# Kernel optimization log

Hardware: AMD Instinct MI355X
Metric: run time of the kernel (lower is better)

Reference implementation:

```python
import jax, jax.numpy as jnp
import numpy as np

HIDDEN = 1024
HEADS = 16
HEAD_DIM = HIDDEN // HEADS
SEQ = 2048
BATCH = 2


def setup_inputs() -> dict:
    key = jax.random.key(0)
    ks = jax.random.split(key, 11)
    s = 1.0 / np.sqrt(HIDDEN)
    inp = {
        'query': jax.random.normal(ks[0], (SEQ, BATCH, HIDDEN), jnp.float32),
        'key': jax.random.normal(ks[1], (SEQ, BATCH, HIDDEN), jnp.float32),
        'value': jax.random.normal(ks[2], (SEQ, BATCH, HIDDEN), jnp.float32),
        'Wq': jax.random.normal(ks[3], (HIDDEN, HIDDEN), jnp.float32) * s,
        'bq': jnp.zeros((HIDDEN,), jnp.float32),
        'Wk': jax.random.normal(ks[4], (HIDDEN, HIDDEN), jnp.float32) * s,
        'bk': jnp.zeros((HIDDEN,), jnp.float32),
        'Wv': jax.random.normal(ks[5], (HIDDEN, HIDDEN), jnp.float32) * s,
        'bv': jnp.zeros((HIDDEN,), jnp.float32),
        'Wo': jax.random.normal(ks[6], (HIDDEN, HIDDEN), jnp.float32) * s,
        'bo': jnp.zeros((HIDDEN,), jnp.float32),
    }
    return inp


def reference(query, key, value, Wq, bq, Wk, bk, Wv, bv, Wo, bo):
    # Linear layers: torch Linear computes x @ W.T + b
    S, B, _ = query.shape
    q = (query @ Wq.T + bq).reshape(S, B, HEADS, HEAD_DIM)
    k = (key @ Wk.T + bk).reshape(S, B, HEADS, HEAD_DIM)
    v = (value @ Wv.T + bv).reshape(S, B, HEADS, HEAD_DIM)
    # -> [B, H, S, D]
    q = jnp.transpose(q, (1, 2, 0, 3))
    k = jnp.transpose(k, (1, 2, 0, 3))
    v = jnp.transpose(v, (1, 2, 0, 3))
    scores = jnp.einsum('bhqd,bhkd->bhqk', q, k) / np.sqrt(HEAD_DIM)
    attn = jax.nn.softmax(scores, axis=-1)  # dropout=0.0 -> identity
    out = jnp.einsum('bhqk,bhkd->bhqd', attn, v)
    out = jnp.transpose(out, (2, 0, 1, 3)).reshape(S, B, HIDDEN)
    out = out @ Wo.T + bo
    return out, attn
```

## Files before the change

### kernel.cpp

```cpp
#include <hip/hip_runtime.h>
#include <hip/hip_bf16.h>
#include <cstdint>
#include <cstddef>

#define SEQLEN 2048
#define NBATCH 2
#define NHEAD  16
#define HDIM   64
#define HID    1024
#define MROWS  4096

typedef __bf16 bf16x8 __attribute__((ext_vector_type(8)));
typedef float f32x4 __attribute__((ext_vector_type(4)));
typedef unsigned short ushort8 __attribute__((ext_vector_type(8)));

#define MFMA16(a, b, c) __builtin_amdgcn_mfma_f32_16x16x32_bf16((a), (b), (c), 0, 0, 0)

#define GLOAD_LDS16(g, l)                                                        \
    __builtin_amdgcn_global_load_lds(                                            \
        (const __attribute__((address_space(1))) void*)(g),                      \
        (__attribute__((address_space(3))) void*)(l), 16, 0, 0)

static __device__ __forceinline__ unsigned int pack_bf16_pair(float lo, float hi) {
    unsigned short a = __builtin_bit_cast(unsigned short, (__bf16)lo);
    unsigned short b = __builtin_bit_cast(unsigned short, (__bf16)hi);
    return ((unsigned int)b << 16) | a;
}

__global__ __launch_bounds__(256) void conv6(
    const float* __restrict__ s0, const float* __restrict__ s1, const float* __restrict__ s2,
    const float* __restrict__ s3, const float* __restrict__ s4, const float* __restrict__ s5,
    unsigned short* __restrict__ Sc)
{
    const int y = blockIdx.y;
    const float* src = (y == 0) ? s0 : (y == 1) ? s1 : (y == 2) ? s2
                     : (y == 3) ? s3 : (y == 4) ? s4 : s5;
    const size_t M1 = 1u << 20;
    unsigned short* dst = (y < 3) ? (Sc + (size_t)y * 4 * M1) : (Sc + 12 * M1 + (size_t)(y - 3) * M1);
    const size_t n = (y < 3) ? 4 * M1 : M1;

    const size_t i = ((size_t)blockIdx.x * 256 + threadIdx.x) * 8;
    if (i >= n) return;
    float4 f0 = *(const float4*)(src + i);
    float4 f1 = *(const float4*)(src + i + 4);
    ushort8 o;
    o[0] = __builtin_bit_cast(unsigned short, (__bf16)f0.x);
    o[1] = __builtin_bit_cast(unsigned short, (__bf16)f0.y);
    o[2] = __builtin_bit_cast(unsigned short, (__bf16)f0.z);
    o[3] = __builtin_bit_cast(unsigned short, (__bf16)f0.w);
    o[4] = __builtin_bit_cast(unsigned short, (__bf16)f1.x);
    o[5] = __builtin_bit_cast(unsigned short, (__bf16)f1.y);
    o[6] = __builtin_bit_cast(unsigned short, (__bf16)f1.z);
    o[7] = __builtin_bit_cast(unsigned short, (__bf16)f1.w);
    *(ushort8*)(dst + i) = o;
}

__global__ __launch_bounds__(256) void wconv(
    const float* __restrict__ Wo, unsigned short* __restrict__ Wob)
{
    const size_t i = ((size_t)blockIdx.x * 256 + threadIdx.x) * 8;
    float4 f0 = *(const float4*)(Wo + i);
    float4 f1 = *(const float4*)(Wo + i + 4);
    ushort8 o;
    o[0] = __builtin_bit_cast(unsigned short, (__bf16)f0.x);
    o[1] = __builtin_bit_cast(unsigned short, (__bf16)f0.y);
    o[2] = __builtin_bit_cast(unsigned short, (__bf16)f0.z);
    o[3] = __builtin_bit_cast(unsigned short, (__bf16)f0.w);
    o[4] = __builtin_bit_cast(unsigned short, (__bf16)f1.x);
    o[5] = __builtin_bit_cast(unsigned short, (__bf16)f1.y);
    o[6] = __builtin_bit_cast(unsigned short, (__bf16)f1.z);
    o[7] = __builtin_bit_cast(unsigned short, (__bf16)f1.w);
    *(ushort8*)(Wob + i) = o;
}

#define GEMM_STAGE(LDSBUF, SRCP)                                                  \
    _Pragma("unroll")                                                             \
    for (int c = 0; c < 4; ++c) {                                                 \
        const int rb = (w << 5) + (c << 3);                                       \
        const int row = rb + (lane >> 3);                                         \
        const unsigned short* src = (SRCP) + (size_t)row * HID + k0               \
                                  + (((lane & 7) ^ ((lane >> 3) & 7)) << 3);      \
        GLOAD_LDS16(src, &LDSBUF[rb * 64]);                                       \
    }

__global__ __launch_bounds__(256) void qkv_gemm(
    const unsigned short* __restrict__ Sc,
    const float* __restrict__ bq, const float* __restrict__ bk, const float* __restrict__ bv,
    unsigned short* __restrict__ Qb, unsigned short* __restrict__ Kb, unsigned short* __restrict__ Vb)
{
    const int z = blockIdx.z;
    const size_t M1 = 1u << 20;
    const unsigned short* A = Sc + (size_t)z * 4 * M1;
    const unsigned short* B = Sc + 12 * M1 + (size_t)z * M1;
    const float* bias = (z == 0) ? bq : (z == 1) ? bk : bv;
    unsigned short* dst = (z == 0) ? Qb : (z == 1) ? Kb : Vb;

    __shared__ unsigned short As[128 * 64];
    __shared__ unsigned short Bs[128 * 64];

    const int t = threadIdx.x, lane = t & 63, w = t >> 6;
    const int wm = w >> 1, wn = w & 1;
    const int bm = blockIdx.x * 128, bn = blockIdx.y * 128;
    const int fr = lane & 15, fg = lane >> 4;

    f32x4 acc[4][4] = {};
    const char* Ac = (const char*)As;
    const char* Bc = (const char*)Bs;

    for (int k0 = 0; k0 < HID; k0 += 64) {
        __syncthreads();
        GEMM_STAGE(As, A + (size_t)bm * HID)
        GEMM_STAGE(Bs, B + (size_t)bn * HID)
        __syncthreads();

        #pragma unroll
        for (int kk = 0; kk < 2; ++kk) {
            bf16x8 a_h[4], b_h[4];
            #pragma unroll
            for (int m = 0; m < 4; ++m) {
                const int row = wm * 64 + m * 16 + fr;
                a_h[m] = *(const bf16x8*)(Ac + (row << 7) + (((kk << 6) | (fg << 4)) ^ ((row & 7) << 4)));
            }
            #pragma unroll
            for (int n = 0; n < 4; ++n) {
                const int row = wn * 64 + n * 16 + fr;
                b_h[n] = *(const bf16x8*)(Bc + (row << 7) + (((kk << 6) | (fg << 4)) ^ ((row & 7) << 4)));
            }
            __builtin_amdgcn_s_setprio(1);
            #pragma unroll
            for (int m = 0; m < 4; ++m)
                #pragma unroll
                for (int n = 0; n < 4; ++n)
                    acc[m][n] = MFMA16(a_h[m], b_h[n], acc[m][n]);
            __builtin_amdgcn_s_setprio(0);
        }
    }

    #pragma unroll
    for (int n = 0; n < 4; ++n) {
        const int gc = bn + wn * 64 + n * 16 + fr;
        const float bb = bias[gc];
        #pragma unroll
        for (int m = 0; m < 4; ++m)
            #pragma unroll
            for (int r = 0; r < 4; ++r) {
                const int gr = bm + wm * 64 + m * 16 + fg * 4 + r;
                *(__bf16*)&dst[(size_t)gr * HID + gc] = (__bf16)(acc[m][n][r] + bb);
            }
    }
}

__global__ __launch_bounds__(256) void vtrans(
    const unsigned short* __restrict__ Vb, unsigned short* __restrict__ Vt)
{
    __shared__ unsigned short T[64][66];
    const int t = threadIdx.x;
    const int s0 = blockIdx.x * 64, h = blockIdx.y, b = blockIdx.z;

    {
        const int s_l = t >> 2, d0 = (t & 3) * 16;
        const unsigned short* src = Vb + (((size_t)(s0 + s_l) * 2 + b) << 10) + (h << 6) + d0;
        *(ushort8*)&T[s_l][d0]     = *(const ushort8*)src;
        *(ushort8*)&T[s_l][d0 + 8] = *(const ushort8*)(src + 8);
    }
    __syncthreads();
    {
        const int d_l = t >> 2, sc = (t & 3) * 16;
        ushort8 o0, o1;
        #pragma unroll
        for (int j = 0; j < 8; ++j) { o0[j] = T[sc + j][d_l]; o1[j] = T[sc + 8 + j][d_l]; }
        unsigned short* dst = Vt + (((size_t)((b << 4) + h) * 64 + d_l) << 11) + s0 + sc;
        *(ushort8*)dst       = o0;
        *(ushort8*)(dst + 8) = o1;
    }
}

__global__ __launch_bounds__(256) void attn2(
    const unsigned short* __restrict__ Qb, const unsigned short* __restrict__ Kb,
    const unsigned short* __restrict__ Vt, float* __restrict__ attn_out,
    unsigned short* __restrict__ Hb)
{
    __shared__ unsigned short Ks[128 * 64];
    __shared__ unsigned short Pl[4 * 32 * 128];

    const int flat = blockIdx.x + (blockIdx.y << 4) + (blockIdx.z << 8);
    const int nf = (flat & 7) * 64 + (flat >> 3);
    const int qblk = nf & 15, h = (nf >> 4) & 15, b = nf >> 8;

    const int t = threadIdx.x, lane = t & 63, w = t >> 6;
    const int fr = lane & 15, fg = lane >> 4;
    const int fg4 = fg << 2, fg16 = fg << 4;
    const int qbase = qblk * 128 + w * 32;
    const float scale = 0.125f;

    bf16x8 qf[2][2];
    #pragma unroll
    for (int mi = 0; mi < 2; ++mi) {
        const int q = qbase + mi * 16 + fr;
        const unsigned short* qp = Qb + (((size_t)q * 2 + b) << 10) + (h << 6);
        qf[mi][0] = *(const bf16x8*)(qp + (fg << 3));
        qf[mi][1] = *(const bf16x8*)(qp + 32 + (fg << 3));
    }

    const char* Ksc = (const char*)Ks;
    char* Plc = (char*)&Pl[w * 4096];

    float lsum[2] = {0.f, 0.f};

    for (int kt = 0; kt < 16; ++kt) {
        __syncthreads();
        #pragma unroll
        for (int c = 0; c < 4; ++c) {
            const int rb = (w << 5) + (c << 3);
            const int row_l = rb + (lane >> 3);
            const unsigned short* src = Kb + (((size_t)((kt << 7) + row_l) * 2 + b) << 10) + (h << 6)
                                         + (((lane & 7) ^ (row_l & 7)) << 3);
            GLOAD_LDS16(src, &Ks[rb * 64]);
        }
        __syncthreads();

        f32x4 s_[2][8] = {};
        __builtin_amdgcn_s_setprio(1);
        #pragma unroll
        for (int n = 0; n < 8; ++n) {
            const int row = (n << 4) + fr;
            const int rx = (row & 7) << 4;
            #pragma unroll
            for (int kk = 0; kk < 2; ++kk) {
                bf16x8 kf = *(const bf16x8*)(Ksc + (row << 7) + (((kk << 6) | fg16) ^ rx));
                s_[0][n] = MFMA16(kf, qf[0][kk], s_[0][n]);
                s_[1][n] = MFMA16(kf, qf[1][kk], s_[1][n]);
            }
        }
        __builtin_amdgcn_s_setprio(0);
        #pragma unroll
        for (int mi = 0; mi < 2; ++mi) {
            float a = 0.f;
            #pragma unroll
            for (int n = 0; n < 8; ++n)
                #pragma unroll
                for (int r = 0; r < 4; ++r)
                    a += __expf(fminf(s_[mi][n][r] * scale, 60.f));
            lsum[mi] += a;
        }
    }

    float inv[2];
    #pragma unroll
    for (int mi = 0; mi < 2; ++mi) {
        float v = lsum[mi];
        v += __shfl_xor(v, 16);
        v += __shfl_xor(v, 32);
        inv[mi] = 1.f / v;
    }

    f32x4 oacc[2][4] = {};
    float* attnB = attn_out + ((size_t)((b << 4) + h) << 22);
    const size_t vhead = (size_t)((b << 4) + h) << 6;

    for (int kt = 0; kt < 16; ++kt) {
        __syncthreads();
        #pragma unroll
        for (int c = 0; c < 4; ++c) {
            const int rb = (w << 5) + (c << 3);
            const int row_l = rb + (lane >> 3);
            const unsigned short* src = Kb + (((size_t)((kt << 7) + row_l) * 2 + b) << 10) + (h << 6)
                                         + (((lane & 7) ^ (row_l & 7)) << 3);
            GLOAD_LDS16(src, &Ks[rb * 64]);
        }
        __syncthreads();

        f32x4 s_[2][8] = {};
        __builtin_amdgcn_s_setprio(1);
        #pragma unroll
        for (int n = 0; n < 8; ++n) {
            const int row = (n << 4) + fr;
            const int rx = (row & 7) << 4;
            #pragma unroll
            for (int kk = 0; kk < 2; ++kk) {
                bf16x8 kf = *(const bf16x8*)(Ksc + (row << 7) + (((kk << 6) | fg16) ^ rx));
                s_[0][n] = MFMA16(kf, qf[0][kk], s_[0][n]);
                s_[1][n] = MFMA16(kf, qf[1][kk], s_[1][n]);
            }
        }
        __builtin_amdgcn_s_setprio(0);

        #pragma unroll
        for (int mi = 0; mi < 2; ++mi) {
            float* ab = attnB + ((size_t)(qbase + mi * 16 + fr) << 11) + (kt << 7) + fg4;
            const int row_l = mi * 16 + fr;
            const int rxl = (row_l & 7) << 4;
            #pragma unroll
            for (int n = 0; n < 8; ++n) {
                f32x4 p;
                #pragma unroll
                for (int r = 0; r < 4; ++r)
                    p[r] = __expf(fminf(s_[mi][n][r] * scale, 60.f)) * inv[mi];
                *(f32x4*)(ab + (n << 4)) = p;
                unsigned int lo = pack_bf16_pair(p[0], p[1]);
                unsigned int hi = pack_bf16_pair(p[2], p[3]);
                uint2 pk = {lo, hi};
                *(uint2*)(Plc + (row_l << 8) + (((n << 5) | (fg << 3)) ^ rxl)) = pk;
            }
        }
        asm volatile("s_waitcnt lgkmcnt(0)" ::: "memory");
        __builtin_amdgcn_sched_barrier(0);

        __builtin_amdgcn_s_setprio(1);
        #pragma unroll
        for (int kk2 = 0; kk2 < 4; ++kk2) {
            const int cb = ((kk2 << 6) | fg16) ^ ((fr & 7) << 4);
            bf16x8 pa0 = *(const bf16x8*)(Plc + (fr << 8) + cb);
            bf16x8 pa1 = *(const bf16x8*)(Plc + ((16 + fr) << 8) + cb);
            #pragma unroll
            for (int n2 = 0; n2 < 4; ++n2) {
                bf16x8 vf = *(const bf16x8*)(Vt + ((vhead + (n2 << 4) + fr) << 11)
                                             + (kt << 7) + (kk2 << 5) + (fg << 3));
                oacc[0][n2] = MFMA16(pa0, vf, oacc[0][n2]);
                oacc[1][n2] = MFMA16(pa1, vf, oacc[1][n2]);
            }
        }
        __builtin_amdgcn_s_setprio(0);
    }

    #pragma unroll
    for (int mi = 0; mi < 2; ++mi)
        #pragma unroll
        for (int n2 = 0; n2 < 4; ++n2)
            #pragma unroll
            for (int r = 0; r < 4; ++r) {
                const int q = qbase + (mi << 4) + fg4 + r;
                *(__bf16*)&Hb[(((size_t)q * 2 + b) << 10) + (h << 6) + (n2 << 4) + fr] =
                    (__bf16)oacc[mi][n2][r];
            }
}

__global__ __launch_bounds__(256) void out_proj(
    const unsigned short* __restrict__ Hb, const unsigned short* __restrict__ Wob,
    const float* __restrict__ bo, float* __restrict__ out)
{
    __shared__ unsigned short As[128 * 64];
    __shared__ unsigned short Bs[128 * 64];

    const int t = threadIdx.x, lane = t & 63, w = t >> 6;
    const int wm = w >> 1, wn = w & 1;
    const int bm = blockIdx.x * 128, bn = blockIdx.y * 128;
    const int fr = lane & 15, fg = lane >> 4;

    f32x4 acc[4][4] = {};
    const char* Ac = (const char*)As;
    const char* Bc = (const char*)Bs;

    for (int k0 = 0; k0 < HID; k0 += 64) {
        __syncthreads();
        GEMM_STAGE(As, Hb + (size_t)bm * HID)
        GEMM_STAGE(Bs, Wob + (size_t)bn * HID)
        __syncthreads();

        #pragma unroll
        for (int kk = 0; kk < 2; ++kk) {
            bf16x8 a_h[4], b_h[4];
            #pragma unroll
            for (int m = 0; m < 4; ++m) {
                const int row = wm * 64 + m * 16 + fr;
                a_h[m] = *(const bf16x8*)(Ac + (row << 7) + (((kk << 6) | (fg << 4)) ^ ((row & 7) << 4)));
            }
            #pragma unroll
            for (int n = 0; n < 4; ++n) {
                const int row = wn * 64 + n * 16 + fr;
                b_h[n] = *(const bf16x8*)(Bc + (row << 7) + (((kk << 6) | (fg << 4)) ^ ((row & 7) << 4)));
            }
            __builtin_amdgcn_s_setprio(1);
            #pragma unroll
            for (int m = 0; m < 4; ++m)
                #pragma unroll
                for (int n = 0; n < 4; ++n)
                    acc[m][n] = MFMA16(a_h[m], b_h[n], acc[m][n]);
            __builtin_amdgcn_s_setprio(0);
        }
    }

    #pragma unroll
    for (int n = 0; n < 4; ++n) {
        const int gc = bn + wn * 64 + n * 16 + fr;
        const float bb = bo[gc];
        #pragma unroll
        for (int m = 0; m < 4; ++m)
            #pragma unroll
            for (int r = 0; r < 4; ++r) {
                const int gr = bm + wm * 64 + m * 16 + fg * 4 + r;
                out[(size_t)gr * HID + gc] = acc[m][n][r] + bb;
            }
    }
}

extern "C" void kernel_launch(void* const* d_in, const int* in_sizes, int n_in,
                              void* d_out, int out_size, void* d_ws, size_t ws_size,
                              hipStream_t stream)
{
    (void)in_sizes; (void)n_in; (void)out_size;

    const float* query = (const float*)d_in[0];
    const float* key   = (const float*)d_in[1];
    const float* value = (const float*)d_in[2];
    const float* bq    = (const float*)d_in[4];
    const float* bk    = (const float*)d_in[6];
    const float* bv    = (const float*)d_in[8];
    const float* Wo    = (const float*)d_in[9];
    const float* bo    = (const float*)d_in[10];

    float* out0 = (float*)d_out;
    float* attn = out0 + (size_t)MROWS * HID;

    if (ws_size < (size_t)32 * 1024 * 1024) return;
    const size_t nbuf = (size_t)MROWS * HID;
    unsigned short* Qb = (unsigned short*)d_ws;
    unsigned short* Kb = Qb + nbuf;
    unsigned short* Vb = Kb + nbuf;
    unsigned short* Vt = Vb + nbuf;
    unsigned short* Hb = Vb;
    unsigned short* Wob = Qb;

    unsigned short* Sc = (unsigned short*)attn;

    conv6<<<dim3(2048, 6), 256, 0, stream>>>(query, key, value,
                                             (const float*)d_in[3], (const float*)d_in[5],
                                             (const float*)d_in[7], Sc);
    qkv_gemm<<<dim3(32, 8, 3), 256, 0, stream>>>(Sc, bq, bk, bv, Qb, Kb, Vb);
    vtrans<<<dim3(32, NHEAD, NBATCH), 256, 0, stream>>>(Vb, Vt);
    attn2<<<dim3(16, NHEAD, NBATCH), 256, 0, stream>>>(Qb, Kb, Vt, attn, Hb);
    wconv<<<dim3(512), 256, 0, stream>>>(Wo, Wob);
    out_proj<<<dim3(32, 8), 256, 0, stream>>>(Hb, Wob, bo, out0);
}
```

Baseline: 326.6 us.

## Double-buffer LDS in GEMMs and attention, fold softmax normalization into exp2

The QKV and output-projection GEMMs now use a double-buffered LDS pipeline with a K-step of 32. The load for the next K slice is issued before computing on the current one, with vmcnt waits in place of full syncthreads pairs. The attention kernel double-buffers its K tiles the same way and replaces expf with an exp2 that carries a pre-scaled constant. It also folds the 1/sum normalization into the exponent as a log2 offset, writes the attention matrix with nontemporal stores, and halves the P scratch by processing one 16-row half at a time. The aim is to overlap global loads with MFMA work and cut the exp and division cost, at the price of more barriers per iteration and a dropped overflow clamp.

```diff
diff --git a/kernel.cpp b/kernel.cpp
--- a/kernel.cpp
+++ b/kernel.cpp
@@ -20,6 +20,10 @@
     __builtin_amdgcn_global_load_lds(                                            \
         (const __attribute__((address_space(1))) void*)(g),                      \
         (__attribute__((address_space(3))) void*)(l), 16, 0, 0)
+
+#define SBAR() __builtin_amdgcn_s_barrier()
+#define SCHED_FENCE() __builtin_amdgcn_sched_barrier(0)
+#define WAIT_VMCNT(n) asm volatile("s_waitcnt vmcnt(" #n ")" ::: "memory")
 
 static __device__ __forceinline__ unsigned int pack_bf16_pair(float lo, float hi) {
     unsigned short a = __builtin_bit_cast(unsigned short, (__bf16)lo);
@@ -73,14 +77,46 @@
     *(ushort8*)(Wob + i) = o;
 }
 
-#define GEMM_STAGE(LDSBUF, SRCP)                                                  \
-    _Pragma("unroll")                                                             \
-    for (int c = 0; c < 4; ++c) {                                                 \
-        const int rb = (w << 5) + (c << 3);                                       \
-        const int row = rb + (lane >> 3);                                         \
-        const unsigned short* src = (SRCP) + (size_t)row * HID + k0               \
-                                  + (((lane & 7) ^ ((lane >> 3) & 7)) << 3);      \
-        GLOAD_LDS16(src, &LDSBUF[rb * 64]);                                       \
+#define GSTAGE32(DSTARR, SRCP, k0v)                                              \
+    _Pragma("unroll")                                                            \
+    for (int c_ = 0; c_ < 2; ++c_) {                                             \
+        const int row_ = (c_ << 6) + (threadIdx.x >> 2);                         \
+        const unsigned short* gs_ = (SRCP) + (size_t)row_ * HID + (k0v)          \
+            + ((((int)threadIdx.x & 3) ^ ((row_ >> 1) & 3)) << 3);               \
+        GLOAD_LDS16(gs_, &(DSTARR)[((c_ << 6) + (((int)threadIdx.x >> 6) << 4)) * 32]); \
+    }
+
+#define GEMM_BODY(ApT, BpT)                                                      \
+    GSTAGE32(As[0], ApT, 0);                                                     \
+    GSTAGE32(Bs[0], BpT, 0);                                                     \
+    for (int it = 0; it < 32; ++it) {                                            \
+        SBAR();                                                                  \
+        const int k1 = ((it + 1) & 31) << 5;                                     \
+        GSTAGE32(As[(it + 1) & 1], ApT, k1);                                     \
+        GSTAGE32(Bs[(it + 1) & 1], BpT, k1);                                     \
+        WAIT_VMCNT(8);                                                           \
+        SBAR();                                                                  \
+        SCHED_FENCE();                                                           \
+        const char* Ac = (const char*)As[it & 1];                                \
+        const char* Bc = (const char*)Bs[it & 1];                                \
+        bf16x8 a_h[4], b_h[4];                                                   \
+        _Pragma("unroll")                                                        \
+        for (int m = 0; m < 4; ++m) {                                            \
+            const int row = wm * 64 + m * 16 + fr;                               \
+            a_h[m] = *(const bf16x8*)(Ac + (row << 6) + ((fg ^ ((row >> 1) & 3)) << 4)); \
+        }                                                                        \
+        _Pragma("unroll")                                                        \
+        for (int n = 0; n < 4; ++n) {                                            \
+            const int row = wn * 64 + n * 16 + fr;                               \
+            b_h[n] = *(const bf16x8*)(Bc + (row << 6) + ((fg ^ ((row >> 1) & 3)) << 4)); \
+        }                                                                        \
+        __builtin_amdgcn_s_setprio(1);                                           \
+        _Pragma("unroll")                                                        \
+        for (int m = 0; m < 4; ++m)                                              \
+            _Pragma("unroll")                                                    \
+            for (int n = 0; n < 4; ++n)                                          \
+                acc[m][n] = MFMA16(a_h[m], b_h[n], acc[m][n]);                   \
+        __builtin_amdgcn_s_setprio(0);                                           \
     }
 
 __global__ __launch_bounds__(256) void qkv_gemm(
@@ -95,46 +131,19 @@
     const float* bias = (z == 0) ? bq : (z == 1) ? bk : bv;
     unsigned short* dst = (z == 0) ? Qb : (z == 1) ? Kb : Vb;
 
-    __shared__ unsigned short As[128 * 64];
-    __shared__ unsigned short Bs[128 * 64];
+    __shared__ unsigned short As[2][128 * 32];
+    __shared__ unsigned short Bs[2][128 * 32];
 
     const int t = threadIdx.x, lane = t & 63, w = t >> 6;
     const int wm = w >> 1, wn = w & 1;
     const int bm = blockIdx.x * 128, bn = blockIdx.y * 128;
     const int fr = lane & 15, fg = lane >> 4;
 
+    const unsigned short* Ap = A + (size_t)bm * HID;
+    const unsigned short* Bp = B + (size_t)bn * HID;
+
     f32x4 acc[4][4] = {};
-    const char* Ac = (const char*)As;
-    const char* Bc = (const char*)Bs;
-
-    for (int k0 = 0; k0 < HID; k0 += 64) {
-        __syncthreads();
-        GEMM_STAGE(As, A + (size_t)bm * HID)
-        GEMM_STAGE(Bs, B + (size_t)bn * HID)
-        __syncthreads();
-
-        #pragma unroll
-        for (int kk = 0; kk < 2; ++kk) {
-            bf16x8 a_h[4], b_h[4];
-            #pragma unroll
-            for (int m = 0; m < 4; ++m) {
-                const int row = wm * 64 + m * 16 + fr;
-                a_h[m] = *(const bf16x8*)(Ac + (row << 7) + (((kk << 6) | (fg << 4)) ^ ((row & 7) << 4)));
-            }
-            #pragma unroll
-            for (int n = 0; n < 4; ++n) {
-                const int row = wn * 64 + n * 16 + fr;
-                b_h[n] = *(const bf16x8*)(Bc + (row << 7) + (((kk << 6) | (fg << 4)) ^ ((row & 7) << 4)));
-            }
-            __builtin_amdgcn_s_setprio(1);
-            #pragma unroll
-            for (int m = 0; m < 4; ++m)
-                #pragma unroll
-                for (int n = 0; n < 4; ++n)
-                    acc[m][n] = MFMA16(a_h[m], b_h[n], acc[m][n]);
-            __builtin_amdgcn_s_setprio(0);
-        }
-    }
+    GEMM_BODY(Ap, Bp)
 
     #pragma unroll
     for (int n = 0; n < 4; ++n) {
@@ -175,13 +184,26 @@
     }
 }
 
+#define STAGE_K(ktv, bufsel)                                                     \
+    {                                                                            \
+        const int kti_ = (ktv) & 15;                                             \
+        _Pragma("unroll")                                                        \
+        for (int c_ = 0; c_ < 4; ++c_) {                                         \
+            const int rb_ = (w << 5) + (c_ << 3);                                \
+            const int rl_ = rb_ + (lane >> 3);                                   \
+            const unsigned short* ks_ = Kb + (((size_t)((kti_ << 7) + rl_) * 2 + b) << 10) \
+                + (h << 6) + (((lane & 7) ^ (rl_ & 7)) << 3);                    \
+            GLOAD_LDS16(ks_, &Ks[bufsel][rb_ * 64]);                             \
+        }                                                                        \
+    }
+
 __global__ __launch_bounds__(256) void attn2(
     const unsigned short* __restrict__ Qb, const unsigned short* __restrict__ Kb,
     const unsigned short* __restrict__ Vt, float* __restrict__ attn_out,
     unsigned short* __restrict__ Hb)
 {
-    __shared__ unsigned short Ks[128 * 64];
-    __shared__ unsigned short Pl[4 * 32 * 128];
+    __shared__ unsigned short Ks[2][128 * 64];
+    __shared__ unsigned short Pl[4][16 * 128];
 
     const int flat = blockIdx.x + (blockIdx.y << 4) + (blockIdx.z << 8);
     const int nf = (flat & 7) * 64 + (flat >> 3);
@@ -191,7 +213,7 @@
     const int fr = lane & 15, fg = lane >> 4;
     const int fg4 = fg << 2, fg16 = fg << 4;
     const int qbase = qblk * 128 + w * 32;
-    const float scale = 0.125f;
+    const float c_exp = 0.18033688011112042f;
 
     bf16x8 qf[2][2];
     #pragma unroll
@@ -202,23 +224,18 @@
         qf[mi][1] = *(const bf16x8*)(qp + 32 + (fg << 3));
     }
 
-    const char* Ksc = (const char*)Ks;
-    char* Plc = (char*)&Pl[w * 4096];
-
+    char* Plc = (char*)&Pl[w][0];
     float lsum[2] = {0.f, 0.f};
 
+    STAGE_K(0, 0);
     for (int kt = 0; kt < 16; ++kt) {
-        __syncthreads();
-        #pragma unroll
-        for (int c = 0; c < 4; ++c) {
-            const int rb = (w << 5) + (c << 3);
-            const int row_l = rb + (lane >> 3);
-            const unsigned short* src = Kb + (((size_t)((kt << 7) + row_l) * 2 + b) << 10) + (h << 6)
-                                         + (((lane & 7) ^ (row_l & 7)) << 3);
-            GLOAD_LDS16(src, &Ks[rb * 64]);
-        }
-        __syncthreads();
-
+        SBAR();
+        STAGE_K(kt + 1, (kt + 1) & 1);
+        WAIT_VMCNT(4);
+        SBAR();
+        SCHED_FENCE();
+
+        const char* Kc = (const char*)Ks[kt & 1];
         f32x4 s_[2][8] = {};
         __builtin_amdgcn_s_setprio(1);
         #pragma unroll
@@ -227,12 +244,13 @@
             const int rx = (row & 7) << 4;
             #pragma unroll
             for (int kk = 0; kk < 2; ++kk) {
-                bf16x8 kf = *(const bf16x8*)(Ksc + (row << 7) + (((kk << 6) | fg16) ^ rx));
+                bf16x8 kf = *(const bf16x8*)(Kc + (row << 7) + (((kk << 6) | fg16) ^ rx));
                 s_[0][n] = MFMA16(kf, qf[0][kk], s_[0][n]);
                 s_[1][n] = MFMA16(kf, qf[1][kk], s_[1][n]);
             }
         }
         __builtin_amdgcn_s_setprio(0);
+
         #pragma unroll
         for (int mi = 0; mi < 2; ++mi) {
             float a = 0.f;
@@ -240,18 +258,18 @@
             for (int n = 0; n < 8; ++n)
                 #pragma unroll
                 for (int r = 0; r < 4; ++r)
-                    a += __expf(fminf(s_[mi][n][r] * scale, 60.f));
+                    a += exp2f(s_[mi][n][r] * c_exp);
             lsum[mi] += a;
         }
     }
 
-    float inv[2];
+    float li[2];
     #pragma unroll
     for (int mi = 0; mi < 2; ++mi) {
         float v = lsum[mi];
         v += __shfl_xor(v, 16);
         v += __shfl_xor(v, 32);
-        inv[mi] = 1.f / v;
+        li[mi] = -__log2f(v);
     }
 
     f32x4 oacc[2][4] = {};
@@ -259,17 +277,13 @@
     const size_t vhead = (size_t)((b << 4) + h) << 6;
 
     for (int kt = 0; kt < 16; ++kt) {
-        __syncthreads();
-        #pragma unroll
-        for (int c = 0; c < 4; ++c) {
-            const int rb = (w << 5) + (c << 3);
-            const int row_l = rb + (lane >> 3);
-            const unsigned short* src = Kb + (((size_t)((kt << 7) + row_l) * 2 + b) << 10) + (h << 6)
-                                         + (((lane & 7) ^ (row_l & 7)) << 3);
-            GLOAD_LDS16(src, &Ks[rb * 64]);
-        }
-        __syncthreads();
-
+        SBAR();
+        STAGE_K(kt + 1, (kt + 1) & 1);
+        WAIT_VMCNT(4);
+        SBAR();
+        SCHED_FENCE();
+
+        const char* Kc = (const char*)Ks[kt & 1];
         f32x4 s_[2][8] = {};
         __builtin_amdgcn_s_setprio(1);
         #pragma unroll
@@ -278,49 +292,45 @@
             const int rx = (row & 7) << 4;
             #pragma unroll
             for (int kk = 0; kk < 2; ++kk) {
-                bf16x8 kf = *(const bf16x8*)(Ksc + (row << 7) + (((kk << 6) | fg16) ^ rx));
+                bf16x8 kf = *(const bf16x8*)(Kc + (row << 7) + (((kk << 6) | fg16) ^ rx));
                 s_[0][n] = MFMA16(kf, qf[0][kk], s_[0][n]);
                 s_[1][n] = MFMA16(kf, qf[1][kk], s_[1][n]);
             }
         }
         __builtin_amdgcn_s_setprio(0);
 
+        const int rxl = (fr & 7) << 4;
         #pragma unroll
         for (int mi = 0; mi < 2; ++mi) {
-            float* ab = attnB + ((size_t)(qbase + mi * 16 + fr) << 11) + (kt << 7) + fg4;
-            const int row_l = mi * 16 + fr;
-            const int rxl = (row_l & 7) << 4;
+            float* ab = attnB + ((size_t)(qbase + (mi << 4) + fr) << 11) + (kt << 7) + fg4;
             #pragma unroll
             for (int n = 0; n < 8; ++n) {
                 f32x4 p;
                 #pragma unroll
                 for (int r = 0; r < 4; ++r)
-                    p[r] = __expf(fminf(s_[mi][n][r] * scale, 60.f)) * inv[mi];
-                *(f32x4*)(ab + (n << 4)) = p;
-                unsigned int lo = pack_bf16_pair(p[0], p[1]);
-                unsigned int hi = pack_bf16_pair(p[2], p[3]);
-                uint2 pk = {lo, hi};
-                *(uint2*)(Plc + (row_l << 8) + (((n << 5) | (fg << 3)) ^ rxl)) = pk;
-            }
+                    p[r] = exp2f(__builtin_fmaf(s_[mi][n][r], c_exp, li[mi]));
+                __builtin_nontemporal_store(p, (f32x4*)(ab + (n << 4)));
+                uint2 pk;
+                pk.x = pack_bf16_pair(p[0], p[1]);
+                pk.y = pack_bf16_pair(p[2], p[3]);
+                *(uint2*)(Plc + (fr << 8) + (((n << 5) | (fg << 3)) ^ rxl)) = pk;
+            }
+            asm volatile("s_waitcnt lgkmcnt(0)" ::: "memory");
+            SCHED_FENCE();
+
+            __builtin_amdgcn_s_setprio(1);
+            #pragma unroll
+            for (int kk2 = 0; kk2 < 4; ++kk2) {
+                bf16x8 pa = *(const bf16x8*)(Plc + (fr << 8) + (((kk2 << 6) | fg16) ^ rxl));
+                #pragma unroll
+                for (int n2 = 0; n2 < 4; ++n2) {
+                    bf16x8 vf = *(const bf16x8*)(Vt + ((vhead + (n2 << 4) + fr) << 11)
+                                                 + (kt << 7) + (kk2 << 5) + (fg << 3));
+                    oacc[mi][n2] = MFMA16(pa, vf, oacc[mi][n2]);
+                }
+            }
+            __builtin_amdgcn_s_setprio(0);
         }
-        asm volatile("s_waitcnt lgkmcnt(0)" ::: "memory");
-        __builtin_amdgcn_sched_barrier(0);
-
-        __builtin_amdgcn_s_setprio(1);
-        #pragma unroll
-        for (int kk2 = 0; kk2 < 4; ++kk2) {
-            const int cb = ((kk2 << 6) | fg16) ^ ((fr & 7) << 4);
-            bf16x8 pa0 = *(const bf16x8*)(Plc + (fr << 8) + cb);
-            bf16x8 pa1 = *(const bf16x8*)(Plc + ((16 + fr) << 8) + cb);
-            #pragma unroll
-            for (int n2 = 0; n2 < 4; ++n2) {
-                bf16x8 vf = *(const bf16x8*)(Vt + ((vhead + (n2 << 4) + fr) << 11)
-                                             + (kt << 7) + (kk2 << 5) + (fg << 3));
-                oacc[0][n2] = MFMA16(pa0, vf, oacc[0][n2]);
-                oacc[1][n2] = MFMA16(pa1, vf, oacc[1][n2]);
-            }
-        }
-        __builtin_amdgcn_s_setprio(0);
     }
 
     #pragma unroll
@@ -339,46 +349,19 @@
     const unsigned short* __restrict__ Hb, const unsigned short* __restrict__ Wob,
     const float* __restrict__ bo, float* __restrict__ out)
 {
-    __shared__ unsigned short As[128 * 64];
-    __shared__ unsigned short Bs[128 * 64];
+    __shared__ unsigned short As[2][128 * 32];
+    __shared__ unsigned short Bs[2][128 * 32];
 
     const int t = threadIdx.x, lane = t & 63, w = t >> 6;
     const int wm = w >> 1, wn = w & 1;
     const int bm = blockIdx.x * 128, bn = blockIdx.y * 128;
     const int fr = lane & 15, fg = lane >> 4;
 
+    const unsigned short* Ap = Hb + (size_t)bm * HID;
+    const unsigned short* Bp = Wob + (size_t)bn * HID;
+
     f32x4 acc[4][4] = {};
-    const char* Ac = (const char*)As;
-    const char* Bc = (const char*)Bs;
-
-    for (int k0 = 0; k0 < HID; k0 += 64) {
-        __syncthreads();
-        GEMM_STAGE(As, Hb + (size_t)bm * HID)
-        GEMM_STAGE(Bs, Wob + (size_t)bn * HID)
-        __syncthreads();
-
-        #pragma unroll
-        for (int kk = 0; kk < 2; ++kk) {
-            bf16x8 a_h[4], b_h[4];
-            #pragma unroll
-            for (int m = 0; m < 4; ++m) {
-                const int row = wm * 64 + m * 16 + fr;
-                a_h[m] = *(const bf16x8*)(Ac + (row << 7) + (((kk << 6) | (fg << 4)) ^ ((row & 7) << 4)));
-            }
-            #pragma unroll
-            for (int n = 0; n < 4; ++n) {
-                const int row = wn * 64 + n * 16 + fr;
-                b_h[n] = *(const bf16x8*)(Bc + (row << 7) + (((kk << 6) | (fg << 4)) ^ ((row & 7) << 4)));
-            }
-            __builtin_amdgcn_s_setprio(1);
-            #pragma unroll
-            for (int m = 0; m < 4; ++m)
-                #pragma unroll
-                for (int n = 0; n < 4; ++n)
-                    acc[m][n] = MFMA16(a_h[m], b_h[n], acc[m][n]);
-            __builtin_amdgcn_s_setprio(0);
-        }
-    }
+    GEMM_BODY(Ap, Bp)
 
     #pragma unroll
     for (int n = 0; n < 4; ++n) {
```

Result: faster. 319.0 us (median of 2 runs) (-2.3%).

## Double-buffer K tiles in attention, fold softmax normalisation into exp2, fuse Wo conversion

Applied to the files above, without the earlier changes.

The attention kernel now double-buffers the K tile in LDS and prefetches the next tile while computing the current one, replacing two barriers per iteration with a single wait and barrier. Softmax uses exp2 with a prescaled constant and subtracts log2 of the row sum inside an fma, which removes the clamp and the multiply by the inverse. The P-times-V step processes one 16-row slice at a time, halving the P staging buffer. The separate Wo fp32-to-bf16 conversion kernel is dropped and the conversion now happens inside the out_proj load stage, which saves a launch but re-reads and re-converts fp32 weights in every block and uses synchronous loads instead of async LDS loads.

```diff
diff --git a/kernel.cpp b/kernel.cpp
--- a/kernel.cpp
+++ b/kernel.cpp
@@ -20,6 +20,11 @@
     __builtin_amdgcn_global_load_lds(                                            \
         (const __attribute__((address_space(1))) void*)(g),                      \
         (__attribute__((address_space(3))) void*)(l), 16, 0, 0)
+
+#define SBAR() __builtin_amdgcn_s_barrier()
+#define SCHED_FENCE() __builtin_amdgcn_sched_barrier(0)
+#define WAIT_VMCNT0() asm volatile("s_waitcnt vmcnt(0)" ::: "memory")
+#define WAIT_LGKM0()  asm volatile("s_waitcnt lgkmcnt(0)" ::: "memory")
 
 static __device__ __forceinline__ unsigned int pack_bf16_pair(float lo, float hi) {
     unsigned short a = __builtin_bit_cast(unsigned short, (__bf16)lo);
@@ -55,24 +60,6 @@
     *(ushort8*)(dst + i) = o;
 }
 
-__global__ __launch_bounds__(256) void wconv(
-    const float* __restrict__ Wo, unsigned short* __restrict__ Wob)
-{
-    const size_t i = ((size_t)blockIdx.x * 256 + threadIdx.x) * 8;
-    float4 f0 = *(const float4*)(Wo + i);
-    float4 f1 = *(const float4*)(Wo + i + 4);
-    ushort8 o;
-    o[0] = __builtin_bit_cast(unsigned short, (__bf16)f0.x);
-    o[1] = __builtin_bit_cast(unsigned short, (__bf16)f0.y);
-    o[2] = __builtin_bit_cast(unsigned short, (__bf16)f0.z);
-    o[3] = __builtin_bit_cast(unsigned short, (__bf16)f0.w);
-    o[4] = __builtin_bit_cast(unsigned short, (__bf16)f1.x);
-    o[5] = __builtin_bit_cast(unsigned short, (__bf16)f1.y);
-    o[6] = __builtin_bit_cast(unsigned short, (__bf16)f1.z);
-    o[7] = __builtin_bit_cast(unsigned short, (__bf16)f1.w);
-    *(ushort8*)(Wob + i) = o;
-}
-
 #define GEMM_STAGE(LDSBUF, SRCP)                                                  \
     _Pragma("unroll")                                                             \
     for (int c = 0; c < 4; ++c) {                                                 \
@@ -83,6 +70,9 @@
         GLOAD_LDS16(src, &LDSBUF[rb * 64]);                                       \
     }
 
+#define FRAG_AT(BUFC, rowv, kkv)                                                  \
+    (*(const bf16x8*)((BUFC) + ((rowv) << 7) + ((((kkv) << 6) | (fg << 4)) ^ (((rowv) & 7) << 4))))
+
 __global__ __launch_bounds__(256) void qkv_gemm(
     const unsigned short* __restrict__ Sc,
     const float* __restrict__ bq, const float* __restrict__ bk, const float* __restrict__ bv,
@@ -117,15 +107,9 @@
         for (int kk = 0; kk < 2; ++kk) {
             bf16x8 a_h[4], b_h[4];
             #pragma unroll
-            for (int m = 0; m < 4; ++m) {
-                const int row = wm * 64 + m * 16 + fr;
-                a_h[m] = *(const bf16x8*)(Ac + (row << 7) + (((kk << 6) | (fg << 4)) ^ ((row & 7) << 4)));
-            }
-            #pragma unroll
-            for (int n = 0; n < 4; ++n) {
-                const int row = wn * 64 + n * 16 + fr;
-                b_h[n] = *(const bf16x8*)(Bc + (row << 7) + (((kk << 6) | (fg << 4)) ^ ((row & 7) << 4)));
-            }
+            for (int m = 0; m < 4; ++m) a_h[m] = FRAG_AT(Ac, wm * 64 + m * 16 + fr, kk);
+            #pragma unroll
+            for (int n = 0; n < 4; ++n) b_h[n] = FRAG_AT(Bc, wn * 64 + n * 16 + fr, kk);
             __builtin_amdgcn_s_setprio(1);
             #pragma unroll
             for (int m = 0; m < 4; ++m)
@@ -175,13 +159,26 @@
     }
 }
 
+#define STAGE_K(ktv, bufsel)                                                     \
+    {                                                                            \
+        const int kti_ = (ktv) & 15;                                             \
+        _Pragma("unroll")                                                        \
+        for (int c_ = 0; c_ < 4; ++c_) {                                         \
+            const int rb_ = (w << 5) + (c_ << 3);                                \
+            const int rl_ = rb_ + (lane >> 3);                                   \
+            const unsigned short* ks_ = Kb + (((size_t)((kti_ << 7) + rl_) * 2 + b) << 10) \
+                + (h << 6) + (((lane & 7) ^ (rl_ & 7)) << 3);                    \
+            GLOAD_LDS16(ks_, &Ks[bufsel][rb_ * 64]);                             \
+        }                                                                        \
+    }
+
 __global__ __launch_bounds__(256) void attn2(
     const unsigned short* __restrict__ Qb, const unsigned short* __restrict__ Kb,
     const unsigned short* __restrict__ Vt, float* __restrict__ attn_out,
     unsigned short* __restrict__ Hb)
 {
-    __shared__ unsigned short Ks[128 * 64];
-    __shared__ unsigned short Pl[4 * 32 * 128];
+    __shared__ unsigned short Ks[2][128 * 64];
+    __shared__ unsigned short Pl[4][16 * 128];
 
     const int flat = blockIdx.x + (blockIdx.y << 4) + (blockIdx.z << 8);
     const int nf = (flat & 7) * 64 + (flat >> 3);
@@ -191,7 +188,7 @@
     const int fr = lane & 15, fg = lane >> 4;
     const int fg4 = fg << 2, fg16 = fg << 4;
     const int qbase = qblk * 128 + w * 32;
-    const float scale = 0.125f;
+    const float c_exp = 0.18033688011112042f;
 
     bf16x8 qf[2][2];
     #pragma unroll
@@ -202,23 +199,16 @@
         qf[mi][1] = *(const bf16x8*)(qp + 32 + (fg << 3));
     }
 
-    const char* Ksc = (const char*)Ks;
-    char* Plc = (char*)&Pl[w * 4096];
-
+    char* Plc = (char*)&Pl[w][0];
     float lsum[2] = {0.f, 0.f};
 
+    STAGE_K(0, 0);
+    WAIT_VMCNT0();
+    SBAR();
     for (int kt = 0; kt < 16; ++kt) {
-        __syncthreads();
-        #pragma unroll
-        for (int c = 0; c < 4; ++c) {
-            const int rb = (w << 5) + (c << 3);
-            const int row_l = rb + (lane >> 3);
-            const unsigned short* src = Kb + (((size_t)((kt << 7) + row_l) * 2 + b) << 10) + (h << 6)
-                                         + (((lane & 7) ^ (row_l & 7)) << 3);
-            GLOAD_LDS16(src, &Ks[rb * 64]);
-        }
-        __syncthreads();
-
+        STAGE_K(kt + 1, (kt + 1) & 1);
+
+        const char* Kc = (const char*)Ks[kt & 1];
         f32x4 s_[2][8] = {};
         __builtin_amdgcn_s_setprio(1);
         #pragma unroll
@@ -227,12 +217,13 @@
             const int rx = (row & 7) << 4;
             #pragma unroll
             for (int kk = 0; kk < 2; ++kk) {
-                bf16x8 kf = *(const bf16x8*)(Ksc + (row << 7) + (((kk << 6) | fg16) ^ rx));
+                bf16x8 kf = *(const bf16x8*)(Kc + (row << 7) + (((kk << 6) | fg16) ^ rx));
                 s_[0][n] = MFMA16(kf, qf[0][kk], s_[0][n]);
                 s_[1][n] = MFMA16(kf, qf[1][kk], s_[1][n]);
             }
         }
         __builtin_amdgcn_s_setprio(0);
+
         #pragma unroll
         for (int mi = 0; mi < 2; ++mi) {
             float a = 0.f;
@@ -240,18 +231,21 @@
             for (int n = 0; n < 8; ++n)
                 #pragma unroll
                 for (int r = 0; r < 4; ++r)
-                    a += __expf(fminf(s_[mi][n][r] * scale, 60.f));
+                    a += exp2f(s_[mi][n][r] * c_exp);
             lsum[mi] += a;
         }
-    }
-
-    float inv[2];
+
+        WAIT_VMCNT0();
+        SBAR();
+    }
+
+    float li[2];
     #pragma unroll
     for (int mi = 0; mi < 2; ++mi) {
         float v = lsum[mi];
         v += __shfl_xor(v, 16);
         v += __shfl_xor(v, 32);
-        inv[mi] = 1.f / v;
+        li[mi] = -__log2f(v);
     }
 
     f32x4 oacc[2][4] = {};
@@ -259,17 +253,9 @@
     const size_t vhead = (size_t)((b << 4) + h) << 6;
 
     for (int kt = 0; kt < 16; ++kt) {
-        __syncthreads();
-        #pragma unroll
-        for (int c = 0; c < 4; ++c) {
-            const int rb = (w << 5) + (c << 3);
-            const int row_l = rb + (lane >> 3);
-            const unsigned short* src = Kb + (((size_t)((kt << 7) + row_l) * 2 + b) << 10) + (h << 6)
-                                         + (((lane & 7) ^ (row_l & 7)) << 3);
-            GLOAD_LDS16(src, &Ks[rb * 64]);
-        }
-        __syncthreads();
-
+        STAGE_K(kt + 1, (kt + 1) & 1);
+
+        const char* Kc = (const char*)Ks[kt & 1];
         f32x4 s_[2][8] = {};
         __builtin_amdgcn_s_setprio(1);
         #pragma unroll
@@ -278,49 +264,48 @@
             const int rx = (row & 7) << 4;
             #pragma unroll
             for (int kk = 0; kk < 2; ++kk) {
-                bf16x8 kf = *(const bf16x8*)(Ksc + (row << 7) + (((kk << 6) | fg16) ^ rx));
+                bf16x8 kf = *(const bf16x8*)(Kc + (row << 7) + (((kk << 6) | fg16) ^ rx));
                 s_[0][n] = MFMA16(kf, qf[0][kk], s_[0][n]);
                 s_[1][n] = MFMA16(kf, qf[1][kk], s_[1][n]);
             }
         }
         __builtin_amdgcn_s_setprio(0);
 
+        const int rxl = (fr & 7) << 4;
         #pragma unroll
         for (int mi = 0; mi < 2; ++mi) {
-            float* ab = attnB + ((size_t)(qbase + mi * 16 + fr) << 11) + (kt << 7) + fg4;
-            const int row_l = mi * 16 + fr;
-            const int rxl = (row_l & 7) << 4;
+            float* ab = attnB + ((size_t)(qbase + (mi << 4) + fr) << 11) + (kt << 7) + fg4;
             #pragma unroll
             for (int n = 0; n < 8; ++n) {
                 f32x4 p;
                 #pragma unroll
                 for (int r = 0; r < 4; ++r)
-                    p[r] = __expf(fminf(s_[mi][n][r] * scale, 60.f)) * inv[mi];
+                    p[r] = exp2f(__builtin_fmaf(s_[mi][n][r], c_exp, li[mi]));
                 *(f32x4*)(ab + (n << 4)) = p;
-                unsigned int lo = pack_bf16_pair(p[0], p[1]);
-                unsigned int hi = pack_bf16_pair(p[2], p[3]);
-                uint2 pk = {lo, hi};
-                *(uint2*)(Plc + (row_l << 8) + (((n << 5) | (fg << 3)) ^ rxl)) = pk;
-            }
-        }
-        asm volatile("s_waitcnt lgkmcnt(0)" ::: "memory");
-        __builtin_amdgcn_sched_barrier(0);
-
-        __builtin_amdgcn_s_setprio(1);
-        #pragma unroll
-        for (int kk2 = 0; kk2 < 4; ++kk2) {
-            const int cb = ((kk2 << 6) | fg16) ^ ((fr & 7) << 4);
-            bf16x8 pa0 = *(const bf16x8*)(Plc + (fr << 8) + cb);
-            bf16x8 pa1 = *(const bf16x8*)(Plc + ((16 + fr) << 8) + cb);
-            #pragma unroll
-            for (int n2 = 0; n2 < 4; ++n2) {
-                bf16x8 vf = *(const bf16x8*)(Vt + ((vhead + (n2 << 4) + fr) << 11)
-                                             + (kt << 7) + (kk2 << 5) + (fg << 3));
-                oacc[0][n2] = MFMA16(pa0, vf, oacc[0][n2]);
-                oacc[1][n2] = MFMA16(pa1, vf, oacc[1][n2]);
-            }
-        }
-        __builtin_amdgcn_s_setprio(0);
+                uint2 pk;
+                pk.x = pack_bf16_pair(p[0], p[1]);
+                pk.y = pack_bf16_pair(p[2], p[3]);
+                *(uint2*)(Plc + (fr << 8) + (((n << 5) | (fg << 3)) ^ rxl)) = pk;
+            }
+            WAIT_LGKM0();
+            SCHED_FENCE();
+
+            __builtin_amdgcn_s_setprio(1);
+            #pragma unroll
+            for (int kk2 = 0; kk2 < 4; ++kk2) {
+                bf16x8 pa = *(const bf16x8*)(Plc + (fr << 8) + (((kk2 << 6) | fg16) ^ rxl));
+                #pragma unroll
+                for (int n2 = 0; n2 < 4; ++n2) {
+                    bf16x8 vf = *(const bf16x8*)(Vt + ((vhead + (n2 << 4) + fr) << 11)
+                                                 + (kt << 7) + (kk2 << 5) + (fg << 3));
+                    oacc[mi][n2] = MFMA16(pa, vf, oacc[mi][n2]);
+                }
+            }
+            __builtin_amdgcn_s_setprio(0);
+        }
+
+        WAIT_VMCNT0();
+        SBAR();
     }
 
     #pragma unroll
@@ -336,7 +321,7 @@
 }
 
 __global__ __launch_bounds__(256) void out_proj(
-    const unsigned short* __restrict__ Hb, const unsigned short* __restrict__ Wob,
+    const unsigned short* __restrict__ Hb, const float* __restrict__ Wo,
     const float* __restrict__ bo, float* __restrict__ out)
 {
     __shared__ unsigned short As[128 * 64];
@@ -350,26 +335,41 @@
     f32x4 acc[4][4] = {};
     const char* Ac = (const char*)As;
     const char* Bc = (const char*)Bs;
+    char* Bw = (char*)Bs;
+
+    const int brow = t >> 1, bhalf = t & 1;
 
     for (int k0 = 0; k0 < HID; k0 += 64) {
         __syncthreads();
         GEMM_STAGE(As, Hb + (size_t)bm * HID)
-        GEMM_STAGE(Bs, Wob + (size_t)bn * HID)
+        {
+            const float* src = Wo + (size_t)(bn + brow) * HID + k0 + bhalf * 32;
+            #pragma unroll
+            for (int c = 0; c < 4; ++c) {
+                float4 f0 = *(const float4*)(src + c * 8);
+                float4 f1 = *(const float4*)(src + c * 8 + 4);
+                ushort8 o;
+                o[0] = __builtin_bit_cast(unsigned short, (__bf16)f0.x);
+                o[1] = __builtin_bit_cast(unsigned short, (__bf16)f0.y);
+                o[2] = __builtin_bit_cast(unsigned short, (__bf16)f0.z);
+                o[3] = __builtin_bit_cast(unsigned short, (__bf16)f0.w);
+                o[4] = __builtin_bit_cast(unsigned short, (__bf16)f1.x);
+                o[5] = __builtin_bit_cast(unsigned short, (__bf16)f1.y);
+                o[6] = __builtin_bit_cast(unsigned short, (__bf16)f1.z);
+                o[7] = __builtin_bit_cast(unsigned short, (__bf16)f1.w);
+                const int cslot = bhalf * 4 + c;
+                *(ushort8*)(Bw + (brow << 7) + ((cslot << 4) ^ ((brow & 7) << 4))) = o;
+            }
+        }
         __syncthreads();
 
         #pragma unroll
         for (int kk = 0; kk < 2; ++kk) {
             bf16x8 a_h[4], b_h[4];
             #pragma unroll
-            for (int m = 0; m < 4; ++m) {
-                const int row = wm * 64 + m * 16 + fr;
-                a_h[m] = *(const bf16x8*)(Ac + (row << 7) + (((kk << 6) | (fg << 4)) ^ ((row & 7) << 4)));
-            }
-            #pragma unroll
-            for (int n = 0; n < 4; ++n) {
-                const int row = wn * 64 + n * 16 + fr;
-                b_h[n] = *(const bf16x8*)(Bc + (row << 7) + (((kk << 6) | (fg << 4)) ^ ((row & 7) << 4)));
-            }
+            for (int m = 0; m < 4; ++m) a_h[m] = FRAG_AT(Ac, wm * 64 + m * 16 + fr, kk);
+            #pragma unroll
+            for (int n = 0; n < 4; ++n) b_h[n] = FRAG_AT(Bc, wn * 64 + n * 16 + fr, kk);
             __builtin_amdgcn_s_setprio(1);
             #pragma unroll
             for (int m = 0; m < 4; ++m)
@@ -419,7 +419,6 @@
     unsigned short* Vb = Kb + nbuf;
     unsigned short* Vt = Vb + nbuf;
     unsigned short* Hb = Vb;
-    unsigned short* Wob = Qb;
 
     unsigned short* Sc = (unsigned short*)attn;
 
@@ -429,6 +428,5 @@
     qkv_gemm<<<dim3(32, 8, 3), 256, 0, stream>>>(Sc, bq, bk, bv, Qb, Kb, Vb);
     vtrans<<<dim3(32, NHEAD, NBATCH), 256, 0, stream>>>(Vb, Vt);
     attn2<<<dim3(16, NHEAD, NBATCH), 256, 0, stream>>>(Qb, Kb, Vt, attn, Hb);
-    wconv<<<dim3(512), 256, 0, stream>>>(Wo, Wob);
-    out_proj<<<dim3(32, 8), 256, 0, stream>>>(Hb, Wob, bo, out0);
-}
+    out_proj<<<dim3(32, 8), 256, 0, stream>>>(Hb, Wo, bo, out0);
+}
```

Result: slower. 399.0 us (+22.2%).
